# Optimization experiments

Hardware: AMD Instinct MI355X
Metric: run time of the kernel (lower is better)

## Reference

```python
import jax, jax.numpy as jnp
import numpy as np

B, S, E = 2, 2048, 2048
H, KVH = 16, 4
D = E // H            # 128
N_REP = H // KVH      # 4


def setup_inputs() -> dict:
    key = jax.random.key(0)
    ks = jax.random.split(key, 5)
    x = jax.random.normal(ks[0], (B, S, E), dtype=jnp.float32)
    # kaiming-normal-ish linear weights, torch layout [out_features, in_features]
    wq_w = jax.random.normal(ks[1], (H * D, E), dtype=jnp.float32) * (2.0 / E) ** 0.5
    wk_w = jax.random.normal(ks[2], (KVH * D, E), dtype=jnp.float32) * (2.0 / E) ** 0.5
    wv_w = jax.random.normal(ks[3], (KVH * D, E), dtype=jnp.float32) * (2.0 / E) ** 0.5
    wo_w = jax.random.normal(ks[4], (E, E), dtype=jnp.float32) * (2.0 / E) ** 0.5
    # standard RoPE frequencies: theta = 10000
    inv_freq = 1.0 / (10000.0 ** (np.arange(0, D, 2, dtype=np.float32) / D))  # [D/2]
    t = np.arange(S, dtype=np.float32)
    ang = np.outer(t, inv_freq)  # [S, D/2]
    freqs_cos = jnp.asarray(np.cos(ang), dtype=jnp.float32)
    freqs_sin = jnp.asarray(np.sin(ang), dtype=jnp.float32)
    return {"x": x, "wq_w": wq_w, "wk_w": wk_w, "wv_w": wv_w, "wo_w": wo_w,
            "freqs_cos": freqs_cos, "freqs_sin": freqs_sin, "start_pos": 0}


def _rope(t, cos, sin):
    # t: [B, S, h, D]; cos/sin: [S, D/2] -> complex multiply on (even, odd) pairs
    tr = t.reshape(*t.shape[:-1], -1, 2)
    xr, xi = tr[..., 0], tr[..., 1]
    c = cos[None, :, None, :]
    s = sin[None, :, None, :]
    orr = xr * c - xi * s
    oi = xr * s + xi * c
    return jnp.stack([orr, oi], axis=-1).reshape(t.shape)


def reference(x, wq_w, wk_w, wv_w, wo_w, freqs_cos, freqs_sin, start_pos):
    b, s, e = x.shape
    q = jnp.einsum('bse,fe->bsf', x, wq_w).reshape(b, s, H, D)
    k = jnp.einsum('bse,fe->bsf', x, wk_w).reshape(b, s, KVH, D)
    v = jnp.einsum('bse,fe->bsf', x, wv_w).reshape(b, s, KVH, D)
    q = _rope(q, freqs_cos, freqs_sin)
    k = _rope(k, freqs_cos, freqs_sin)
    # faithful to torch .repeat(1,1,n_rep,1): TILE kv heads -> head h uses kv head h % KVH
    k = jnp.tile(k, (1, 1, N_REP, 1))  # [b, s, H, D]
    v = jnp.tile(v, (1, 1, N_REP, 1))
    q = q.transpose(0, 2, 1, 3)  # [b, H, s, D]
    k = k.transpose(0, 2, 1, 3)
    v = v.transpose(0, 2, 1, 3)
    scores = jnp.einsum('bhqd,bhkd->bhqk', q, k) * (1.0 / D ** 0.5)
    causal = jnp.tril(jnp.ones((s, s), dtype=bool))
    scores = jnp.where(causal[None, None], scores, -jnp.inf)
    attn = jax.nn.softmax(scores, axis=-1)
    out = jnp.einsum('bhqk,bhkd->bhqd', attn, v)
    out = out.transpose(0, 2, 1, 3).reshape(b, s, e)
    return jnp.einsum('bse,fe->bsf', out, wo_w)
```

## Files before the change

kernel.cpp:

```cpp
#include <hip/hip_runtime.h>
#include <hip/hip_bf16.h>

typedef unsigned short u16;
typedef unsigned int u32;
typedef short bf16x8 __attribute__((ext_vector_type(8)));
typedef float f32x4 __attribute__((ext_vector_type(4)));

#define MFMA_BF16 __builtin_amdgcn_mfma_f32_16x16x32_bf16

#define B_   2
#define S_   2048
#define E_   2048
#define H_   16
#define KVH_ 4
#define D_   128
#define M_   (B_ * S_)
#define NQKV 3072
#define SCALE_ 0.08838834764831845f

__device__ __forceinline__ float b2f(u16 u) {
    union { u32 i; float f; } x; x.i = ((u32)u) << 16; return x.f;
}
__device__ __forceinline__ u16 f2b(float f) {
    __hip_bfloat16 h = __float2bfloat16(f);
    return *reinterpret_cast<u16*>(&h);
}

__device__ __forceinline__ void async16(const u16* g, u16* l) {
    __builtin_amdgcn_global_load_lds(
        (const __attribute__((address_space(1))) void*)g,
        (__attribute__((address_space(3))) void*)l, 16, 0, 0);
}

__device__ __forceinline__ uint4 pack8(const float* p) {
    float4 a = *reinterpret_cast<const float4*>(p);
    float4 b = *reinterpret_cast<const float4*>(p + 4);
    union { uint4 v; u16 h[8]; } pk;
    pk.h[0] = f2b(a.x); pk.h[1] = f2b(a.y); pk.h[2] = f2b(a.z); pk.h[3] = f2b(a.w);
    pk.h[4] = f2b(b.x); pk.h[5] = f2b(b.y); pk.h[6] = f2b(b.z); pk.h[7] = f2b(b.w);
    return pk.v;
}

__global__ __launch_bounds__(256)
void conv4(const float* __restrict__ s0, u16* __restrict__ d0, int n0,
           const float* __restrict__ s1, u16* __restrict__ d1, int n1,
           const float* __restrict__ s2, u16* __restrict__ d2, int n2,
           const float* __restrict__ s3, u16* __restrict__ d3) {
    int bid = blockIdx.x;
    const float* s; u16* d; size_t base;
    if (bid < n0)                { s = s0; d = d0; base = (size_t)bid * 2048; }
    else if (bid < n0 + n1)      { s = s1; d = d1; base = (size_t)(bid - n0) * 2048; }
    else if (bid < n0 + n1 + n2) { s = s2; d = d2; base = (size_t)(bid - n0 - n1) * 2048; }
    else                         { s = s3; d = d3; base = (size_t)(bid - n0 - n1 - n2) * 2048; }
    size_t i = base + (size_t)threadIdx.x * 8;
    *reinterpret_cast<uint4*>(d + i) = pack8(s + i);
}

template <int NREP>
__device__ __forceinline__ void gemm_core(const u16* __restrict__ Ag, int m0,
                                          const u16* const (&Bp)[NREP],
                                          u16* lds, f32x4 (&acc)[8][NREP]) {
    constexpr int BUFSZ = 16384 + NREP * 64 * 64;
    const int tid = threadIdx.x, wave = tid >> 6, lane = tid & 63;
    const int l15 = lane & 15, quad = lane >> 4;
    const int wm = wave & 1, wn = wave >> 1;

    const f32x4 zero4 = {0.f, 0.f, 0.f, 0.f};
    #pragma unroll
    for (int i = 0; i < 8; ++i)
        #pragma unroll
        for (int j = 0; j < NREP; ++j) acc[i][j] = zero4;

    const u16* Ap[4];
    #pragma unroll
    for (int j = 0; j < 4; ++j) {
        int tA = wave * 4 + j;
        Ap[j] = Ag + (size_t)(m0 + (tA >> 1) * 16 + l15) * E_
                   + (tA & 1) * 32 + quad * 8;
    }

    auto stage = [&](int p, int kt) {
        #pragma unroll
        for (int j = 0; j < 4; ++j)
            async16(Ap[j] + kt, &lds[p * BUFSZ + (wave * 4 + j) * 512]);
        #pragma unroll
        for (int j = 0; j < NREP; ++j)
            async16(Bp[j] + kt, &lds[p * BUFSZ + 16384 + (wave * NREP + j) * 512]);
    };

    stage(0, 0);

    int p = 0;
    for (int kt = 0; kt < E_; kt += 64) {
        __builtin_amdgcn_s_barrier();
        if (kt + 64 < E_) {
            stage(p ^ 1, kt + 64);
            if constexpr (NREP == 2)
                asm volatile("s_waitcnt vmcnt(6)" ::: "memory");
            else
                asm volatile("s_waitcnt vmcnt(7)" ::: "memory");
        } else {
            asm volatile("s_waitcnt vmcnt(0)" ::: "memory");
        }
        __builtin_amdgcn_sched_barrier(0);
        __builtin_amdgcn_s_barrier();
        __builtin_amdgcn_sched_barrier(0);

        #pragma unroll
        for (int kb = 0; kb < 2; ++kb) {
            bf16x8 bfr[NREP];
            #pragma unroll
            for (int ni = 0; ni < NREP; ++ni)
                bfr[ni] = *reinterpret_cast<const bf16x8*>(
                    &lds[p * BUFSZ + 16384 +
                         ((((wn * NREP + ni) << 1) | kb) << 9) + lane * 8]);
            bf16x8 af[4];
            #pragma unroll
            for (int i = 0; i < 4; ++i)
                af[i] = *reinterpret_cast<const bf16x8*>(
                    &lds[p * BUFSZ + ((((wm * 8 + i) << 1) | kb) << 9) + lane * 8]);
            __builtin_amdgcn_s_setprio(1);
            #pragma unroll
            for (int mi = 0; mi < 4; ++mi)
                #pragma unroll
                for (int ni = 0; ni < NREP; ++ni)
                    acc[mi][ni] = MFMA_BF16(af[mi], bfr[ni], acc[mi][ni], 0, 0, 0);
            __builtin_amdgcn_s_setprio(0);
            #pragma unroll
            for (int i = 0; i < 4; ++i)
                af[i] = *reinterpret_cast<const bf16x8*>(
                    &lds[p * BUFSZ + ((((wm * 8 + 4 + i) << 1) | kb) << 9) + lane * 8]);
            __builtin_amdgcn_s_setprio(1);
            #pragma unroll
            for (int mi = 0; mi < 4; ++mi)
                #pragma unroll
                for (int ni = 0; ni < NREP; ++ni)
                    acc[4 + mi][ni] = MFMA_BF16(af[mi], bfr[ni], acc[4 + mi][ni], 0, 0, 0);
            __builtin_amdgcn_s_setprio(0);
        }
        p ^= 1;
    }
}

__global__ __launch_bounds__(512, 2)
void qkv_rope_gemm(const u16* __restrict__ xb, const u16* __restrict__ wqb,
                   const u16* __restrict__ wkb, const u16* __restrict__ wvb,
                   const float* __restrict__ fc, const float* __restrict__ fs,
                   u16* __restrict__ Qr, u16* __restrict__ Kr,
                   u16* __restrict__ Vr) {
    __shared__ __align__(16) u16 lds[2 * (16384 + 192 * 64)];
    const int tid = threadIdx.x, wave = tid >> 6, lane = tid & 63;
    const int l15 = lane & 15, quad = lane >> 4;
    const int m0 = blockIdx.y * 256, n0 = blockIdx.x * 192;

    const u16* Bp[3];
    #pragma unroll
    for (int j = 0; j < 3; ++j) {
        int tB = wave * 3 + j;
        int n = n0 + (tB >> 1) * 16 + l15;
        const u16* base; int nl;
        if (n < 2048)      { base = wqb; nl = n; }
        else if (n < 2560) { base = wkb; nl = n - 2048; }
        else               { base = wvb; nl = n - 2560; }
        Bp[j] = base + (size_t)nl * E_ + (tB & 1) * 32 + quad * 8;
    }

    f32x4 acc[8][3];
    gemm_core<3>(xb, m0, Bp, lds, acc);

    const int wm = wave & 1, wn = wave >> 1;
    const int mb_ = m0 + wm * 128, nbase = n0 + wn * 48;
    #pragma unroll
    for (int mi = 0; mi < 8; ++mi)
        #pragma unroll
        for (int ni = 0; ni < 3; ++ni)
            #pragma unroll
            for (int r = 0; r < 4; ++r) {
                int m = mb_ + mi * 16 + quad * 4 + r;
                int n = nbase + ni * 16 + l15;
                int b = m >> 11, s = m & 2047;
                float v = acc[mi][ni][r];
                float other = __shfl_xor(v, 1);
                if (n < 2560) {
                    int d = n & 127;
                    int fi = s * 64 + (d >> 1);
                    float c  = fc[fi];
                    float sn = fs[fi];
                    v = (n & 1) ? (other * sn + v * c) : (v * c - other * sn);
                }
                if (n < 2048) {
                    Qr[((size_t)(b * H_ + (n >> 7)) * S_ + s) * D_ + (n & 127)] = f2b(v);
                } else if (n < 2560) {
                    int kh = (n - 2048) >> 7;
                    Kr[((size_t)(b * KVH_ + kh) * S_ + s) * D_ + (n & 127)] = f2b(v);
                } else {
                    int kh = (n - 2560) >> 7;
                    Vr[((size_t)(b * KVH_ + kh) * S_ + s) * D_ + (n & 127)] = f2b(v);
                }
            }
}

__global__ __launch_bounds__(256)
void transpose_v(const u16* __restrict__ Vr, u16* __restrict__ VrT) {
    __shared__ u16 t[64][72];
    const int tid = threadIdx.x;
    const int s0 = blockIdx.x * 64, d0 = blockIdx.y * 64, g = blockIdx.z;
    const u16* src = Vr + (size_t)g * S_ * D_;
    u16* dst = VrT + (size_t)g * D_ * S_;
    #pragma unroll
    for (int i = 0; i < 2; ++i) {
        int c = tid + i * 256;
        int r = c >> 3, cc = (c & 7) * 8;
        *reinterpret_cast<uint4*>(&t[r][cc]) =
            *reinterpret_cast<const uint4*>(src + (size_t)(s0 + r) * D_ + d0 + cc);
    }
    __syncthreads();
    #pragma unroll
    for (int i = 0; i < 2; ++i) {
        int c = tid + i * 256;
        int r = c >> 3, cc = (c & 7) * 8;
        u16 tmp[8];
        #pragma unroll
        for (int e = 0; e < 8; ++e) tmp[e] = t[cc + e][r];
        *reinterpret_cast<uint4*>(dst + (size_t)(d0 + r) * S_ + s0 + cc) =
            *reinterpret_cast<const uint4*>(tmp);
    }
}

__global__ __launch_bounds__(1024, 4)
void flash2(const u16* __restrict__ Qr, const u16* __restrict__ Kr,
            const u16* __restrict__ VrT, u16* __restrict__ AO) {
    __shared__ __align__(16) u16 Ks[2][2][8192];
    __shared__ __align__(16) u16 Vs[2][2][8192];
    const int tid = threadIdx.x, wave = tid >> 6, lane = tid & 63;
    const int grp = wave >> 3, gw = wave & 7;
    const int l15 = lane & 15, quad = lane >> 4;
    const int lin = blockIdx.x;
    const int qt  = 15 - (lin >> 5);
    const int sub = lin & 31;
    const int h = sub & 15, b = sub >> 4;
    const int kvh = h & 3;
    const u16* Qb = Qr + (size_t)(b * H_ + h) * S_ * D_;
    const u16* Kb = Kr + (size_t)(b * KVH_ + kvh) * S_ * D_;
    const u16* Vb = VrT + (size_t)(b * KVH_ + kvh) * D_ * S_;
    const int q0 = qt * 128 + gw * 16;
    const int qg = q0 + l15;

    bf16x8 bq[4];
    #pragma unroll
    for (int kk = 0; kk < 4; ++kk)
        bq[kk] = *reinterpret_cast<const bf16x8*>(
            Qb + (size_t)qg * D_ + kk * 32 + quad * 8);

    f32x4 o[8];
    const f32x4 zero4 = {0.f, 0.f, 0.f, 0.f};
    #pragma unroll
    for (int i = 0; i < 8; ++i) o[i] = zero4;
    float m_i = -__builtin_inff(), l_i = 0.f;

    const int nt = qt + 1;
    const int tbase = grp ? nt : 0;
    const int f0 = gw * 2, f1 = gw * 2 + 1;
    const u16* kp0 = Kb + (size_t)tbase * 64 * D_ +
        (size_t)((f0 >> 2) * 16 + l15) * D_ + (f0 & 3) * 32 + quad * 8;
    const u16* kp1 = Kb + (size_t)tbase * 64 * D_ +
        (size_t)((f1 >> 2) * 16 + l15) * D_ + (f1 & 3) * 32 + quad * 8;
    const u16* vp0 = Vb + (size_t)tbase * 64 +
        (size_t)((f0 >> 1) * 16 + l15) * S_ + (f0 & 1) * 32 + quad * 8;
    const u16* vp1 = Vb + (size_t)tbase * 64 +
        (size_t)((f1 >> 1) * 16 + l15) * S_ + (f1 & 1) * 32 + quad * 8;

    async16(kp0, &Ks[grp][0][f0 * 512]);
    async16(kp1, &Ks[grp][0][f1 * 512]);
    async16(vp0, &Vs[grp][0][f0 * 512]);
    async16(vp1, &Vs[grp][0][f1 * 512]);

    int p = 0;
    for (int i = 0; i < nt; ++i) {
        __builtin_amdgcn_s_barrier();
        if (i + 1 < nt) {
            size_t ko = (size_t)(i + 1) * 64 * D_;
            size_t vo = (size_t)(i + 1) * 64;
            async16(kp0 + ko, &Ks[grp][p ^ 1][f0 * 512]);
            async16(kp1 + ko, &Ks[grp][p ^ 1][f1 * 512]);
            async16(vp0 + vo, &Vs[grp][p ^ 1][f0 * 512]);
            async16(vp1 + vo, &Vs[grp][p ^ 1][f1 * 512]);
            asm volatile("s_waitcnt vmcnt(4)" ::: "memory");
        } else {
            asm volatile("s_waitcnt vmcnt(0)" ::: "memory");
        }
        __builtin_amdgcn_sched_barrier(0);
        __builtin_amdgcn_s_barrier();
        __builtin_amdgcn_sched_barrier(0);

        const int kvbase = (tbase + i) * 64;
        if (q0 + 15 >= kvbase) {
            f32x4 st[4];
            #pragma unroll
            for (int kb = 0; kb < 4; ++kb) st[kb] = zero4;
            __builtin_amdgcn_s_setprio(1);
            #pragma unroll
            for (int kk = 0; kk < 4; ++kk)
                #pragma unroll
                for (int kb = 0; kb < 4; ++kb) {
                    bf16x8 ak = *reinterpret_cast<const bf16x8*>(
                        &Ks[grp][p][(((kb << 2) | kk) << 9) + lane * 8]);
                    st[kb] = MFMA_BF16(ak, bq[kk], st[kb], 0, 0, 0);
                }
            __builtin_amdgcn_s_setprio(0);

            float mx = -__builtin_inff();
            if (kvbase + 63 > q0) {
                #pragma unroll
                for (int kb = 0; kb < 4; ++kb)
                    #pragma unroll
                    for (int r = 0; r < 4; ++r) {
                        float s = st[kb][r] * SCALE_;
                        if (kvbase + kb * 16 + quad * 4 + r > qg)
                            s = -__builtin_inff();
                        st[kb][r] = s;
                        mx = fmaxf(mx, s);
                    }
            } else {
                #pragma unroll
                for (int kb = 0; kb < 4; ++kb)
                    #pragma unroll
                    for (int r = 0; r < 4; ++r) {
                        float s = st[kb][r] * SCALE_;
                        st[kb][r] = s;
                        mx = fmaxf(mx, s);
                    }
            }
            mx = fmaxf(mx, __shfl_xor(mx, 16));
            mx = fmaxf(mx, __shfl_xor(mx, 32));
            const bool nodefer = !__all(mx - m_i <= 8.0f);
            float mnew = nodefer ? fmaxf(m_i, mx) : m_i;
            float a = __expf(m_i - mnew);
            float sum = 0.f;
            #pragma unroll
            for (int kb = 0; kb < 4; ++kb)
                #pragma unroll
                for (int r = 0; r < 4; ++r) {
                    float pv = __expf(st[kb][r] - mnew);
                    st[kb][r] = pv;
                    sum += pv;
                }
            sum += __shfl_xor(sum, 16);
            sum += __shfl_xor(sum, 32);
            l_i = l_i * a + sum;
            m_i = mnew;
            if (nodefer) {
                #pragma unroll
                for (int mi = 0; mi < 8; ++mi)
                    #pragma unroll
                    for (int r = 0; r < 4; ++r) o[mi][r] *= a;
            }

            #pragma unroll
            for (int kf = 0; kf < 2; ++kf) {
                u32 pk[4];
                #pragma unroll
                for (int r = 0; r < 4; ++r)
                    pk[r] = (u32)f2b(st[kf * 2 + 0][r]) |
                            ((u32)f2b(st[kf * 2 + 1][r]) << 16);
                bf16x8 bp;
                u16* bh = (u16*)&bp;
                #pragma unroll
                for (int j2 = 0; j2 < 8; ++j2) {
                    int src = ((quad & 1) * 2 + (j2 >> 2)) * 16 + l15;
                    u32 v = __shfl((int)pk[j2 & 3], src);
                    bh[j2] = (lane >= 32) ? (u16)(v >> 16) : (u16)v;
                }
                __builtin_amdgcn_s_setprio(1);
                #pragma unroll
                for (int mi = 0; mi < 8; ++mi) {
                    bf16x8 av = *reinterpret_cast<const bf16x8*>(
                        &Vs[grp][p][(((mi << 1) | kf) << 9) + lane * 8]);
                    o[mi] = MFMA_BF16(av, bp, o[mi], 0, 0, 0);
                }
                __builtin_amdgcn_s_setprio(0);
            }
        }
        p ^= 1;
    }

    float* shf = (float*)&Ks[0][0][0];
    float* shm = (float*)&Vs[0][0][0];
    __syncthreads();
    if (grp == 1) {
        #pragma unroll
        for (int mi = 0; mi < 8; ++mi)
            #pragma unroll
            for (int r = 0; r < 4; ++r)
                shf[((mi << 2) | r) * 512 + gw * 64 + lane] = o[mi][r];
        shm[gw * 64 + lane] = m_i;
        shm[512 + gw * 64 + lane] = l_i;
    }
    __syncthreads();
    if (grp == 0) {
        float m1 = shm[gw * 64 + lane];
        float l1 = shm[512 + gw * 64 + lane];
        float M  = fmaxf(m_i, m1);
        float w0 = __expf(m_i - M), w1 = __expf(m1 - M);
        float inv = 1.0f / (w0 * l_i + w1 * l1);
        size_t base = ((size_t)(b * S_ + qg)) * E_ + h * D_;
        #pragma unroll
        for (int mi = 0; mi < 8; ++mi) {
            u16 w[4];
            #pragma unroll
            for (int r = 0; r < 4; ++r) {
                float ov = w0 * o[mi][r] +
                           w1 * shf[((mi << 2) | r) * 512 + gw * 64 + lane];
                w[r] = f2b(ov * inv);
            }
            *reinterpret_cast<uint2*>(AO + base + mi * 16 + quad * 4) =
                *reinterpret_cast<const uint2*>(w);
        }
    }
}

__global__ __launch_bounds__(512, 2)
void out_proj_gemm(const u16* __restrict__ ao, const u16* __restrict__ wob,
                   float* __restrict__ out) {
    __shared__ __align__(16) u16 lds[2 * (16384 + 128 * 64)];
    const int tid = threadIdx.x, wave = tid >> 6, lane = tid & 63;
    const int l15 = lane & 15, quad = lane >> 4;
    const int m0 = blockIdx.y * 256, n0 = blockIdx.x * 128;

    const u16* Bp[2];
    #pragma unroll
    for (int j = 0; j < 2; ++j) {
        int tB = wave * 2 + j;
        Bp[j] = wob + (size_t)(n0 + (tB >> 1) * 16 + l15) * E_
                    + (tB & 1) * 32 + quad * 8;
    }

    f32x4 acc[8][2];
    gemm_core<2>(ao, m0, Bp, lds, acc);

    const int wm = wave & 1, wn = wave >> 1;
    const int mb_ = m0 + wm * 128, nbase = n0 + wn * 32;
    #pragma unroll
    for (int mi = 0; mi < 8; ++mi)
        #pragma unroll
        for (int ni = 0; ni < 2; ++ni)
            #pragma unroll
            for (int r = 0; r < 4; ++r) {
                int m = mb_ + mi * 16 + quad * 4 + r;
                int n = nbase + ni * 16 + l15;
                out[(size_t)m * E_ + n] = acc[mi][ni][r];
            }
}

extern "C" void kernel_launch(void* const* d_in, const int* in_sizes, int n_in,
                              void* d_out, int out_size, void* d_ws, size_t ws_size,
                              hipStream_t stream) {
    const float* x  = (const float*)d_in[0];
    const float* wq = (const float*)d_in[1];
    const float* wk = (const float*)d_in[2];
    const float* wv = (const float*)d_in[3];
    const float* wo = (const float*)d_in[4];
    const float* fc = (const float*)d_in[5];
    const float* fs = (const float*)d_in[6];
    float* out = (float*)d_out;

    u16* wqb = (u16*)d_ws;
    u16* xb  = wqb + 4194304;
    u16* Qr  = wqb + 12582912;
    u16* Kr  = wqb + 20971520;
    u16* Vr  = wqb + 23068672;
    u16* VrT = wqb;
    u16* wob = wqb;
    u16* AO  = xb;
    u16* wkb = (u16*)d_out;
    u16* wvb = wkb + 1048576;

    conv4<<<7168, 256, 0, stream>>>(x, xb, 4096, wq, wqb, 2048,
                                    wk, wkb, 512, wv, wvb);
    qkv_rope_gemm<<<dim3(NQKV / 192, M_ / 256), 512, 0, stream>>>(
        xb, wqb, wkb, wvb, fc, fs, Qr, Kr, Vr);
    transpose_v<<<dim3(S_ / 64, D_ / 64, B_ * KVH_), 256, 0, stream>>>(Vr, VrT);
    flash2<<<dim3(512), 1024, 0, stream>>>(Qr, Kr, VrT, AO);
    conv4<<<2048, 256, 0, stream>>>(wo, wob, 2048, nullptr, nullptr, 0,
                                    nullptr, nullptr, 0, nullptr, nullptr);
    out_proj_gemm<<<dim3(E_ / 128, M_ / 256), 512, 0, stream>>>(AO, wob, out);
}
```

Measured before the change: 345.1 us.

## Split GEMM main loop into four barrier-synced phases and swizzle blocks across XCDs

The shared GEMM core is restructured into four sub-phases per K-tile. Each phase loads its LDS fragments, issues part of the next tile's global-to-LDS prefetch (A in phase one, B in phase two), then runs an MFMA burst between block barriers. The goal is to interleave loads with matrix math more evenly and keep waves in lockstep. Both GEMM kernels also remap block indices so blocks on the same XCD share A/B tiles, improving L2 reuse. In exchange there are more barriers per iteration, and the swizzle assumes a 16x16 grid.

```diff
diff --git a/kernel.cpp b/kernel.cpp
--- a/kernel.cpp
+++ b/kernel.cpp
@@ -79,67 +79,118 @@
                    + (tA & 1) * 32 + quad * 8;
     }
 
-    auto stage = [&](int p, int kt) {
+    auto stageA = [&](int p, int kt) {
         #pragma unroll
         for (int j = 0; j < 4; ++j)
             async16(Ap[j] + kt, &lds[p * BUFSZ + (wave * 4 + j) * 512]);
+    };
+    auto stageB = [&](int p, int kt) {
         #pragma unroll
         for (int j = 0; j < NREP; ++j)
             async16(Bp[j] + kt, &lds[p * BUFSZ + 16384 + (wave * NREP + j) * 512]);
     };
 
-    stage(0, 0);
+    stageA(0, 0); stageB(0, 0);
+    asm volatile("s_waitcnt vmcnt(0)" ::: "memory");
+    __builtin_amdgcn_sched_barrier(0);
+    __builtin_amdgcn_s_barrier();
 
     int p = 0;
     for (int kt = 0; kt < E_; kt += 64) {
-        __builtin_amdgcn_s_barrier();
-        if (kt + 64 < E_) {
-            stage(p ^ 1, kt + 64);
-            if constexpr (NREP == 2)
-                asm volatile("s_waitcnt vmcnt(6)" ::: "memory");
-            else
-                asm volatile("s_waitcnt vmcnt(7)" ::: "memory");
-        } else {
-            asm volatile("s_waitcnt vmcnt(0)" ::: "memory");
-        }
-        __builtin_amdgcn_sched_barrier(0);
-        __builtin_amdgcn_s_barrier();
-        __builtin_amdgcn_sched_barrier(0);
-
-        #pragma unroll
-        for (int kb = 0; kb < 2; ++kb) {
-            bf16x8 bfr[NREP];
+        const bool pre = (kt + 64 < E_);
+        bf16x8 af[4], bfr[NREP];
+
+        #pragma unroll
+        for (int ni = 0; ni < NREP; ++ni)
+            bfr[ni] = *reinterpret_cast<const bf16x8*>(
+                &lds[p * BUFSZ + 16384 + (((wn * NREP + ni) << 1) << 9) + lane * 8]);
+        #pragma unroll
+        for (int i = 0; i < 4; ++i)
+            af[i] = *reinterpret_cast<const bf16x8*>(
+                &lds[p * BUFSZ + (((wm * 8 + i) << 1) << 9) + lane * 8]);
+        if (pre) stageA(p ^ 1, kt + 64);
+        __builtin_amdgcn_sched_barrier(0);
+        __builtin_amdgcn_s_barrier();
+        asm volatile("s_waitcnt lgkmcnt(0)" ::: "memory");
+        __builtin_amdgcn_sched_barrier(0);
+        __builtin_amdgcn_s_setprio(1);
+        #pragma unroll
+        for (int mi = 0; mi < 4; ++mi)
             #pragma unroll
             for (int ni = 0; ni < NREP; ++ni)
-                bfr[ni] = *reinterpret_cast<const bf16x8*>(
-                    &lds[p * BUFSZ + 16384 +
-                         ((((wn * NREP + ni) << 1) | kb) << 9) + lane * 8]);
-            bf16x8 af[4];
-            #pragma unroll
-            for (int i = 0; i < 4; ++i)
-                af[i] = *reinterpret_cast<const bf16x8*>(
-                    &lds[p * BUFSZ + ((((wm * 8 + i) << 1) | kb) << 9) + lane * 8]);
-            __builtin_amdgcn_s_setprio(1);
-            #pragma unroll
-            for (int mi = 0; mi < 4; ++mi)
-                #pragma unroll
-                for (int ni = 0; ni < NREP; ++ni)
-                    acc[mi][ni] = MFMA_BF16(af[mi], bfr[ni], acc[mi][ni], 0, 0, 0);
-            __builtin_amdgcn_s_setprio(0);
-            #pragma unroll
-            for (int i = 0; i < 4; ++i)
-                af[i] = *reinterpret_cast<const bf16x8*>(
-                    &lds[p * BUFSZ + ((((wm * 8 + 4 + i) << 1) | kb) << 9) + lane * 8]);
-            __builtin_amdgcn_s_setprio(1);
-            #pragma unroll
-            for (int mi = 0; mi < 4; ++mi)
-                #pragma unroll
-                for (int ni = 0; ni < NREP; ++ni)
-                    acc[4 + mi][ni] = MFMA_BF16(af[mi], bfr[ni], acc[4 + mi][ni], 0, 0, 0);
-            __builtin_amdgcn_s_setprio(0);
-        }
+                acc[mi][ni] = MFMA_BF16(af[mi], bfr[ni], acc[mi][ni], 0, 0, 0);
+        __builtin_amdgcn_s_setprio(0);
+        __builtin_amdgcn_sched_barrier(0);
+        __builtin_amdgcn_s_barrier();
+
+        #pragma unroll
+        for (int i = 0; i < 4; ++i)
+            af[i] = *reinterpret_cast<const bf16x8*>(
+                &lds[p * BUFSZ + (((wm * 8 + 4 + i) << 1) << 9) + lane * 8]);
+        if (pre) stageB(p ^ 1, kt + 64);
+        __builtin_amdgcn_sched_barrier(0);
+        __builtin_amdgcn_s_barrier();
+        asm volatile("s_waitcnt lgkmcnt(0)" ::: "memory");
+        __builtin_amdgcn_sched_barrier(0);
+        __builtin_amdgcn_s_setprio(1);
+        #pragma unroll
+        for (int mi = 0; mi < 4; ++mi)
+            #pragma unroll
+            for (int ni = 0; ni < NREP; ++ni)
+                acc[4 + mi][ni] = MFMA_BF16(af[mi], bfr[ni], acc[4 + mi][ni], 0, 0, 0);
+        __builtin_amdgcn_s_setprio(0);
+        __builtin_amdgcn_sched_barrier(0);
+        __builtin_amdgcn_s_barrier();
+
+        #pragma unroll
+        for (int ni = 0; ni < NREP; ++ni)
+            bfr[ni] = *reinterpret_cast<const bf16x8*>(
+                &lds[p * BUFSZ + 16384 + (((((wn * NREP + ni) << 1) | 1)) << 9) + lane * 8]);
+        #pragma unroll
+        for (int i = 0; i < 4; ++i)
+            af[i] = *reinterpret_cast<const bf16x8*>(
+                &lds[p * BUFSZ + (((((wm * 8 + i) << 1) | 1)) << 9) + lane * 8]);
+        __builtin_amdgcn_sched_barrier(0);
+        __builtin_amdgcn_s_barrier();
+        asm volatile("s_waitcnt lgkmcnt(0)" ::: "memory");
+        __builtin_amdgcn_sched_barrier(0);
+        __builtin_amdgcn_s_setprio(1);
+        #pragma unroll
+        for (int mi = 0; mi < 4; ++mi)
+            #pragma unroll
+            for (int ni = 0; ni < NREP; ++ni)
+                acc[mi][ni] = MFMA_BF16(af[mi], bfr[ni], acc[mi][ni], 0, 0, 0);
+        __builtin_amdgcn_s_setprio(0);
+        __builtin_amdgcn_sched_barrier(0);
+        __builtin_amdgcn_s_barrier();
+
+        #pragma unroll
+        for (int i = 0; i < 4; ++i)
+            af[i] = *reinterpret_cast<const bf16x8*>(
+                &lds[p * BUFSZ + (((((wm * 8 + 4 + i) << 1) | 1)) << 9) + lane * 8]);
+        __builtin_amdgcn_sched_barrier(0);
+        __builtin_amdgcn_s_barrier();
+        asm volatile("s_waitcnt lgkmcnt(0)" ::: "memory");
+        __builtin_amdgcn_sched_barrier(0);
+        __builtin_amdgcn_s_setprio(1);
+        #pragma unroll
+        for (int mi = 0; mi < 4; ++mi)
+            #pragma unroll
+            for (int ni = 0; ni < NREP; ++ni)
+                acc[4 + mi][ni] = MFMA_BF16(af[mi], bfr[ni], acc[4 + mi][ni], 0, 0, 0);
+        __builtin_amdgcn_s_setprio(0);
+        asm volatile("s_waitcnt vmcnt(0)" ::: "memory");
+        __builtin_amdgcn_sched_barrier(0);
+        __builtin_amdgcn_s_barrier();
+
         p ^= 1;
     }
+}
+
+__device__ __forceinline__ void xcd_swz16x16(int lin, int& nIdx, int& mIdx) {
+    const int xcd = lin & 7, c = lin >> 3;
+    nIdx = (xcd & 3) * 4 + (c & 3);
+    mIdx = (xcd >> 2) * 8 + (c >> 2);
 }
 
 __global__ __launch_bounds__(512, 2)
@@ -151,7 +202,9 @@
     __shared__ __align__(16) u16 lds[2 * (16384 + 192 * 64)];
     const int tid = threadIdx.x, wave = tid >> 6, lane = tid & 63;
     const int l15 = lane & 15, quad = lane >> 4;
-    const int m0 = blockIdx.y * 256, n0 = blockIdx.x * 192;
+    int nIdx, mIdx;
+    xcd_swz16x16(blockIdx.y * gridDim.x + blockIdx.x, nIdx, mIdx);
+    const int m0 = mIdx * 256, n0 = nIdx * 192;
 
     const u16* Bp[3];
     #pragma unroll
@@ -425,7 +478,9 @@
     __shared__ __align__(16) u16 lds[2 * (16384 + 128 * 64)];
     const int tid = threadIdx.x, wave = tid >> 6, lane = tid & 63;
     const int l15 = lane & 15, quad = lane >> 4;
-    const int m0 = blockIdx.y * 256, n0 = blockIdx.x * 128;
+    int nIdx, mIdx;
+    xcd_swz16x16(blockIdx.y * gridDim.x + blockIdx.x, nIdx, mIdx);
+    const int m0 = mIdx * 256, n0 = nIdx * 128;
 
     const u16* Bp[2];
     #pragma unroll
```

Result: slower. 357.4 us (+3.6%).

## Halve GEMM M-tile to 128 and add XCD-aware block swizzle

Applied to the files above, without the earlier changes.

Both the QKV and output-projection GEMMs shrink their M tile from 256 to 128 rows. This halves the accumulators and LDS per block, doubles the grid size and raises launch_bounds occupancy from 2 to 4 blocks. A swizzle maps linear block IDs so that blocks on the same XCD share neighbouring N/M tiles, aiming to improve L2 reuse. The swizzle hardcodes a 512-block grid (16x32), which fits both launches, but each block now has less operand reuse per tile.

```diff
diff --git a/kernel.cpp b/kernel.cpp
--- a/kernel.cpp
+++ b/kernel.cpp
@@ -59,33 +59,33 @@
 template <int NREP>
 __device__ __forceinline__ void gemm_core(const u16* __restrict__ Ag, int m0,
                                           const u16* const (&Bp)[NREP],
-                                          u16* lds, f32x4 (&acc)[8][NREP]) {
-    constexpr int BUFSZ = 16384 + NREP * 64 * 64;
+                                          u16* lds, f32x4 (&acc)[4][NREP]) {
+    constexpr int BUFSZ = 8192 + NREP * 4096;
     const int tid = threadIdx.x, wave = tid >> 6, lane = tid & 63;
     const int l15 = lane & 15, quad = lane >> 4;
     const int wm = wave & 1, wn = wave >> 1;
 
     const f32x4 zero4 = {0.f, 0.f, 0.f, 0.f};
     #pragma unroll
-    for (int i = 0; i < 8; ++i)
+    for (int i = 0; i < 4; ++i)
         #pragma unroll
         for (int j = 0; j < NREP; ++j) acc[i][j] = zero4;
 
-    const u16* Ap[4];
-    #pragma unroll
-    for (int j = 0; j < 4; ++j) {
-        int tA = wave * 4 + j;
+    const u16* Ap[2];
+    #pragma unroll
+    for (int j = 0; j < 2; ++j) {
+        int tA = wave * 2 + j;
         Ap[j] = Ag + (size_t)(m0 + (tA >> 1) * 16 + l15) * E_
                    + (tA & 1) * 32 + quad * 8;
     }
 
     auto stage = [&](int p, int kt) {
         #pragma unroll
-        for (int j = 0; j < 4; ++j)
-            async16(Ap[j] + kt, &lds[p * BUFSZ + (wave * 4 + j) * 512]);
+        for (int j = 0; j < 2; ++j)
+            async16(Ap[j] + kt, &lds[p * BUFSZ + (wave * 2 + j) * 512]);
         #pragma unroll
         for (int j = 0; j < NREP; ++j)
-            async16(Bp[j] + kt, &lds[p * BUFSZ + 16384 + (wave * NREP + j) * 512]);
+            async16(Bp[j] + kt, &lds[p * BUFSZ + 8192 + (wave * NREP + j) * 512]);
     };
 
     stage(0, 0);
@@ -96,9 +96,9 @@
         if (kt + 64 < E_) {
             stage(p ^ 1, kt + 64);
             if constexpr (NREP == 2)
-                asm volatile("s_waitcnt vmcnt(6)" ::: "memory");
+                asm volatile("s_waitcnt vmcnt(4)" ::: "memory");
             else
-                asm volatile("s_waitcnt vmcnt(7)" ::: "memory");
+                asm volatile("s_waitcnt vmcnt(5)" ::: "memory");
         } else {
             asm volatile("s_waitcnt vmcnt(0)" ::: "memory");
         }
@@ -112,13 +112,13 @@
             #pragma unroll
             for (int ni = 0; ni < NREP; ++ni)
                 bfr[ni] = *reinterpret_cast<const bf16x8*>(
-                    &lds[p * BUFSZ + 16384 +
+                    &lds[p * BUFSZ + 8192 +
                          ((((wn * NREP + ni) << 1) | kb) << 9) + lane * 8]);
             bf16x8 af[4];
             #pragma unroll
             for (int i = 0; i < 4; ++i)
                 af[i] = *reinterpret_cast<const bf16x8*>(
-                    &lds[p * BUFSZ + ((((wm * 8 + i) << 1) | kb) << 9) + lane * 8]);
+                    &lds[p * BUFSZ + ((((wm * 4 + i) << 1) | kb) << 9) + lane * 8]);
             __builtin_amdgcn_s_setprio(1);
             #pragma unroll
             for (int mi = 0; mi < 4; ++mi)
@@ -126,32 +126,29 @@
                 for (int ni = 0; ni < NREP; ++ni)
                     acc[mi][ni] = MFMA_BF16(af[mi], bfr[ni], acc[mi][ni], 0, 0, 0);
             __builtin_amdgcn_s_setprio(0);
-            #pragma unroll
-            for (int i = 0; i < 4; ++i)
-                af[i] = *reinterpret_cast<const bf16x8*>(
-                    &lds[p * BUFSZ + ((((wm * 8 + 4 + i) << 1) | kb) << 9) + lane * 8]);
-            __builtin_amdgcn_s_setprio(1);
-            #pragma unroll
-            for (int mi = 0; mi < 4; ++mi)
-                #pragma unroll
-                for (int ni = 0; ni < NREP; ++ni)
-                    acc[4 + mi][ni] = MFMA_BF16(af[mi], bfr[ni], acc[4 + mi][ni], 0, 0, 0);
-            __builtin_amdgcn_s_setprio(0);
         }
         p ^= 1;
     }
 }
 
-__global__ __launch_bounds__(512, 2)
+__device__ __forceinline__ void xcd_swz512(int lin, int& nIdx, int& mIdx) {
+    const int xcd = lin & 7, c = lin >> 3;
+    nIdx = (xcd & 3) * 4 + (c & 3);
+    mIdx = (xcd >> 2) * 16 + (c >> 2);
+}
+
+__global__ __launch_bounds__(512, 4)
 void qkv_rope_gemm(const u16* __restrict__ xb, const u16* __restrict__ wqb,
                    const u16* __restrict__ wkb, const u16* __restrict__ wvb,
                    const float* __restrict__ fc, const float* __restrict__ fs,
                    u16* __restrict__ Qr, u16* __restrict__ Kr,
                    u16* __restrict__ Vr) {
-    __shared__ __align__(16) u16 lds[2 * (16384 + 192 * 64)];
+    __shared__ __align__(16) u16 lds[2 * (8192 + 12288)];
     const int tid = threadIdx.x, wave = tid >> 6, lane = tid & 63;
     const int l15 = lane & 15, quad = lane >> 4;
-    const int m0 = blockIdx.y * 256, n0 = blockIdx.x * 192;
+    int nIdx, mIdx;
+    xcd_swz512(blockIdx.y * gridDim.x + blockIdx.x, nIdx, mIdx);
+    const int m0 = mIdx * 128, n0 = nIdx * 192;
 
     const u16* Bp[3];
     #pragma unroll
@@ -165,13 +162,13 @@
         Bp[j] = base + (size_t)nl * E_ + (tB & 1) * 32 + quad * 8;
     }
 
-    f32x4 acc[8][3];
+    f32x4 acc[4][3];
     gemm_core<3>(xb, m0, Bp, lds, acc);
 
     const int wm = wave & 1, wn = wave >> 1;
-    const int mb_ = m0 + wm * 128, nbase = n0 + wn * 48;
-    #pragma unroll
-    for (int mi = 0; mi < 8; ++mi)
+    const int mb_ = m0 + wm * 64, nbase = n0 + wn * 48;
+    #pragma unroll
+    for (int mi = 0; mi < 4; ++mi)
         #pragma unroll
         for (int ni = 0; ni < 3; ++ni)
             #pragma unroll
@@ -419,13 +416,15 @@
     }
 }
 
-__global__ __launch_bounds__(512, 2)
+__global__ __launch_bounds__(512, 4)
 void out_proj_gemm(const u16* __restrict__ ao, const u16* __restrict__ wob,
                    float* __restrict__ out) {
-    __shared__ __align__(16) u16 lds[2 * (16384 + 128 * 64)];
+    __shared__ __align__(16) u16 lds[2 * (8192 + 8192)];
     const int tid = threadIdx.x, wave = tid >> 6, lane = tid & 63;
     const int l15 = lane & 15, quad = lane >> 4;
-    const int m0 = blockIdx.y * 256, n0 = blockIdx.x * 128;
+    int nIdx, mIdx;
+    xcd_swz512(blockIdx.y * gridDim.x + blockIdx.x, nIdx, mIdx);
+    const int m0 = mIdx * 128, n0 = nIdx * 128;
 
     const u16* Bp[2];
     #pragma unroll
@@ -435,13 +434,13 @@
                     + (tB & 1) * 32 + quad * 8;
     }
 
-    f32x4 acc[8][2];
+    f32x4 acc[4][2];
     gemm_core<2>(ao, m0, Bp, lds, acc);
 
     const int wm = wave & 1, wn = wave >> 1;
-    const int mb_ = m0 + wm * 128, nbase = n0 + wn * 32;
-    #pragma unroll
-    for (int mi = 0; mi < 8; ++mi)
+    const int mb_ = m0 + wm * 64, nbase = n0 + wn * 32;
+    #pragma unroll
+    for (int mi = 0; mi < 4; ++mi)
         #pragma unroll
         for (int ni = 0; ni < 2; ++ni)
             #pragma unroll
@@ -477,11 +476,11 @@
 
     conv4<<<7168, 256, 0, stream>>>(x, xb, 4096, wq, wqb, 2048,
                                     wk, wkb, 512, wv, wvb);
-    qkv_rope_gemm<<<dim3(NQKV / 192, M_ / 256), 512, 0, stream>>>(
+    qkv_rope_gemm<<<dim3(NQKV / 192, M_ / 128), 512, 0, stream>>>(
         xb, wqb, wkb, wvb, fc, fs, Qr, Kr, Vr);
     transpose_v<<<dim3(S_ / 64, D_ / 64, B_ * KVH_), 256, 0, stream>>>(Vr, VrT);
     flash2<<<dim3(512), 1024, 0, stream>>>(Qr, Kr, VrT, AO);
     conv4<<<2048, 256, 0, stream>>>(wo, wob, 2048, nullptr, nullptr, 0,
                                     nullptr, nullptr, 0, nullptr, nullptr);
-    out_proj_gemm<<<dim3(E_ / 128, M_ / 256), 512, 0, stream>>>(AO, wob, out);
-}
+    out_proj_gemm<<<dim3(E_ / 128, M_ / 128), 512, 0, stream>>>(AO, wob, out);
+}
```

Measured after the change: 357.4 us. 3.6% more time.
